# Performance work log

Hardware: AMD Instinct MI355X
Metric: run time of the kernel (lower is better)

Reference implementation:

```python
import jax, jax.numpy as jnp
import numpy as np

N_NODES = 20000  # number of atoms (scatter target count)


def setup_inputs() -> dict:
    key = jax.random.key(0)
    ks = jax.random.split(key, 7)
    E, F, R, L, O = 640000, 128, 16, 3, 12
    return {
        "m_ji": jax.random.normal(ks[0], (E, F), jnp.float32),
        "rbf_ji": jax.random.normal(ks[1], (E, R), jnp.float32),
        "atom_edge_index": jax.random.randint(ks[2], (2, E), 0, N_NODES, jnp.int64),
        "W_rbf": jax.random.normal(ks[3], (F, R), jnp.float32) * (1.0 / np.sqrt(R)),
        "dense_W": jax.random.normal(ks[4], (L, F, F), jnp.float32) * (1.0 / np.sqrt(F)),
        "dense_b": jax.random.normal(ks[5], (L, F), jnp.float32) * 0.01,
        "W_out": jax.random.normal(ks[6], (O, F), jnp.float32) * (1.0 / np.sqrt(F)),
    }


def reference(m_ji, rbf_ji, atom_edge_index, W_rbf, dense_W, dense_b, W_out):
    # e_ji = lin_rbf(rbf_ji): [E, dim_rbf] @ [dim_rbf, F] -> [E, F]
    e_ji = jnp.einsum("er,fr->ef", rbf_ji, W_rbf)
    # elementwise gate
    message_ji = e_ji * m_ji
    # scatter-add messages onto receiving atoms (index row 1)
    atom_i = jax.ops.segment_sum(message_ji, atom_edge_index[1], num_segments=N_NODES)
    # dense MLP stack with SiLU activation
    num_lin = dense_W.shape[0]
    for idx in range(num_lin):
        atom_i = jax.nn.silu(jnp.einsum("nf,gf->ng", atom_i, dense_W[idx]) + dense_b[idx])
    # final bias-free projection
    return jnp.einsum("nf,of->no", atom_i, W_out)
```

## Files before the change

kernel.cpp:

```cpp
#include <hip/hip_runtime.h>
#include <math.h>

#define F 128
#define R 16
#define O 12
#define NB 32
#define EB 16

__global__ void zero_int_kernel(int* __restrict__ p, int n) {
    int i = blockIdx.x * blockDim.x + threadIdx.x;
    if (i < n) p[i] = 0;
}

__global__ __launch_bounds__(256) void hist_kernel(
    const int* __restrict__ idx, int* __restrict__ cnt, int E)
{
    int i = blockIdx.x * blockDim.x + threadIdx.x;
    int stride = gridDim.x * blockDim.x;
    for (; i < E; i += stride) atomicAdd(&cnt[idx[i]], 1);
}

__global__ __launch_bounds__(1024) void scan_kernel(
    const int* __restrict__ cnt, int* __restrict__ off,
    int* __restrict__ cur, int N, int E)
{
    __shared__ int part[1024];
    int t = threadIdx.x;
    const int per = (N + 1023) / 1024;
    int s0 = t * per;
    int s = 0;
    for (int i = 0; i < per; i++) { int k = s0 + i; if (k < N) s += cnt[k]; }
    part[t] = s;
    __syncthreads();
    for (int d = 1; d < 1024; d <<= 1) {
        int v = (t >= d) ? part[t - d] : 0;
        __syncthreads();
        part[t] += v;
        __syncthreads();
    }
    int run = (t == 0) ? 0 : part[t - 1];
    for (int i = 0; i < per; i++) {
        int k = s0 + i;
        if (k < N) { off[k] = run; cur[k] = run; run += cnt[k]; }
    }
    if (t == 0) off[N] = E;
}

__global__ __launch_bounds__(256) void fill_kernel(
    const int* __restrict__ idx, int* __restrict__ cur,
    int* __restrict__ csr, int E)
{
    int i = blockIdx.x * blockDim.x + threadIdx.x;
    int stride = gridDim.x * blockDim.x;
    for (; i < E; i += stride) {
        int n = idx[i];
        int p = atomicAdd(&cur[n], 1);
        csr[p] = i;
    }
}

__device__ __forceinline__ float dot16(const float4* r, const float4* Wv) {
    float s = 0.f;
    #pragma unroll
    for (int q = 0; q < 4; q++)
        s += r[q].x * Wv[q].x + r[q].y * Wv[q].y + r[q].z * Wv[q].z + r[q].w * Wv[q].w;
    return s;
}

__device__ __forceinline__ void gld_lds16(const float* g, float* l) {
    __builtin_amdgcn_global_load_lds(
        (const __attribute__((address_space(1))) void*)g,
        (__attribute__((address_space(3))) void*)l,
        16, 0, 0);
}

__global__ __launch_bounds__(256) void gather_kernel(
    const float* __restrict__ m, const float* __restrict__ rbf,
    const int* __restrict__ csr, const int* __restrict__ off,
    const float* __restrict__ Wrbf, float* __restrict__ A, int N)
{
    __shared__ float m_buf[4 * EB * F];
    __shared__ float r_buf[4 * EB * R];
    const int lane = threadIdx.x & 63;
    const int w = threadIdx.x >> 6;
    const int n = blockIdx.x * 4 + w;
    if (n >= N) return;

    float* mw = m_buf + w * EB * F;
    float* rw = r_buf + w * EB * R;

    const int f0 = lane << 1;
    float4 W0[4], W1[4];
    #pragma unroll
    for (int q = 0; q < 4; q++) {
        W0[q] = *(const float4*)(Wrbf + (size_t)f0 * R + q * 4);
        W1[q] = *(const float4*)(Wrbf + (size_t)(f0 + 1) * R + q * 4);
    }

    float a0 = 0.f, a1 = 0.f;
    const int jb = off[n], je = off[n + 1];

    for (int j = jb; j < je; j += EB) {
        const int c = (je - j < EB) ? (je - j) : EB;

        asm volatile("s_waitcnt lgkmcnt(0)" ::: "memory");

        #pragma unroll
        for (int k = 0; k < EB / 2; k++) {
            if (2 * k < c) {
                int jj = j + 2 * k + (lane >> 5);
                if (jj > je - 1) jj = je - 1;
                int e = csr[jj];
                gld_lds16(m + (size_t)e * F + ((lane & 31) << 2), mw + k * 2 * F);
            }
        }
        {
            int jj = j + (lane >> 2);
            if (jj > je - 1) jj = je - 1;
            int e = csr[jj];
            gld_lds16(rbf + (size_t)e * R + ((lane & 3) << 2), rw);
        }

        asm volatile("s_waitcnt vmcnt(0)" ::: "memory");

        for (int r = 0; r < c; r++) {
            float2 mv = *(const float2*)(mw + r * F + f0);
            const float4* rr = (const float4*)(rw + r * R);
            float4 rv[4] = { rr[0], rr[1], rr[2], rr[3] };
            a0 += dot16(rv, W0) * mv.x;
            a1 += dot16(rv, W1) * mv.y;
        }
    }

    *(float2*)(A + (size_t)n * F + f0) = make_float2(a0, a1);
}

__global__ __launch_bounds__(256) void mlp_fused(
    const float* __restrict__ A, const float* __restrict__ dW,
    const float* __restrict__ db, const float* __restrict__ Wout,
    float* __restrict__ out, int N)
{
    __shared__ float Ws[F * F];
    __shared__ float act[NB * F];
    int t = threadIdx.x;
    int base = blockIdx.x * NB;
    int j = t & 15, i = t >> 4;

    int  n0[2]; bool ok[2];
    #pragma unroll
    for (int k = 0; k < 2; k++) { n0[k] = base + i + 16 * k; ok[k] = n0[k] < N; }

    for (int l = 0; l < 3; l++) {
        __syncthreads();
        for (int s = t; s < F * F / 4; s += 256) {
            int g = s >> 5, c = s & 31;
            float4 v = *(const float4*)(dW + (size_t)l * F * F + g * F + (c << 2));
            *(float4*)(Ws + g * F + ((c ^ (g & 31)) << 2)) = v;
        }
        __syncthreads();

        float acc[2][8];
        #pragma unroll
        for (int k = 0; k < 2; k++)
            #pragma unroll
            for (int mm = 0; mm < 8; mm++) acc[k][mm] = 0.f;

        for (int c = 0; c < 32; c++) {
            int f = c << 2;
            float4 av[2];
            #pragma unroll
            for (int k = 0; k < 2; k++) {
                if (l == 0)
                    av[k] = ok[k] ? *(const float4*)(A + (size_t)n0[k] * F + f)
                                  : make_float4(0.f, 0.f, 0.f, 0.f);
                else
                    av[k] = *(const float4*)(act + (i + 16 * k) * F + f);
            }
            float4 wv[8];
            #pragma unroll
            for (int mm = 0; mm < 8; mm++) {
                int g = j + 16 * mm;
                wv[mm] = *(const float4*)(Ws + g * F + ((c ^ (g & 31)) << 2));
            }
            #pragma unroll
            for (int k = 0; k < 2; k++)
                #pragma unroll
                for (int mm = 0; mm < 8; mm++)
                    acc[k][mm] += av[k].x * wv[mm].x + av[k].y * wv[mm].y +
                                  av[k].z * wv[mm].z + av[k].w * wv[mm].w;
        }

        #pragma unroll
        for (int mm = 0; mm < 8; mm++) {
            int g = j + 16 * mm;
            float bias = db[l * F + g];
            #pragma unroll
            for (int k = 0; k < 2; k++) {
                float x = acc[k][mm] + bias;
                act[(i + 16 * k) * F + g] = x / (1.f + __expf(-x));
            }
        }
    }

    __syncthreads();
    for (int s = t; s < O * F / 4; s += 256)
        ((float4*)Ws)[s] = ((const float4*)Wout)[s];
    __syncthreads();

    int nl = t >> 3;
    int oq = t & 7;
    int n = base + nl;
    if (n < N) {
        float s0 = 0.f, s1 = 0.f;
        for (int f = 0; f < F; f += 4) {
            float4 a  = *(const float4*)(act + nl * F + f);
            float4 w0 = *(const float4*)(Ws + oq * F + f);
            s0 += a.x * w0.x + a.y * w0.y + a.z * w0.z + a.w * w0.w;
            if (oq < 4) {
                float4 w1 = *(const float4*)(Ws + (8 + oq) * F + f);
                s1 += a.x * w1.x + a.y * w1.y + a.z * w1.z + a.w * w1.w;
            }
        }
        out[(size_t)n * O + oq] = s0;
        if (oq < 4) out[(size_t)n * O + 8 + oq] = s1;
    }
}

extern "C" void kernel_launch(void* const* d_in, const int* in_sizes, int n_in,
                              void* d_out, int out_size, void* d_ws, size_t ws_size,
                              hipStream_t stream)
{
    const float* m    = (const float*)d_in[0];
    const float* rbf  = (const float*)d_in[1];
    const int*   aei  = (const int*)d_in[2];
    const float* Wrbf = (const float*)d_in[3];
    const float* dW   = (const float*)d_in[4];
    const float* db   = (const float*)d_in[5];
    const float* Wout = (const float*)d_in[6];
    float* out = (float*)d_out;

    int E = in_sizes[0] / F;
    int N = out_size / O;

    float* A = (float*)d_ws;
    int* csr = (int*)(A + (size_t)N * F);
    int* cnt = csr + E;
    int* cur = cnt + N;
    int* off = cur + N;

    const int* idx1 = aei + E;

    zero_int_kernel<<<(N + 255) / 256, 256, 0, stream>>>(cnt, N);
    hist_kernel<<<1024, 256, 0, stream>>>(idx1, cnt, E);
    scan_kernel<<<1, 1024, 0, stream>>>(cnt, off, cur, N, E);
    fill_kernel<<<1024, 256, 0, stream>>>(idx1, cur, csr, E);
    gather_kernel<<<(N + 3) / 4, 256, 0, stream>>>(m, rbf, csr, off, Wrbf, A, N);

    mlp_fused<<<(N + NB - 1) / NB, 256, 0, stream>>>(A, dW, db, Wout, out, N);
}
```

Baseline: 743.4 us.

## Double-buffer edge message gathers and load rbf rows via scalar broadcast

The gather kernel now double-buffers the per-wave LDS staging of m rows. The next chunk's CSR indices are read into scalar registers and their async global-to-LDS loads are issued before the current chunk is processed. rbf rows are no longer staged through LDS; each lane loads them directly from uniform addresses, prefetching one row ahead in registers. The chunk size drops to 8 to keep LDS use the same. The aim is to hide gather latency behind compute. The cost is more vector registers, more uniform global loads, and partial vmcnt waits that must match the number of outstanding loads.

```diff
diff --git a/kernel.cpp b/kernel.cpp
--- a/kernel.cpp
+++ b/kernel.cpp
@@ -5,7 +5,7 @@
 #define R 16
 #define O 12
 #define NB 32
-#define EB 16
+#define EB 8
 
 __global__ void zero_int_kernel(int* __restrict__ p, int n) {
     int i = blockIdx.x * blockDim.x + threadIdx.x;
@@ -79,15 +79,13 @@
     const int* __restrict__ csr, const int* __restrict__ off,
     const float* __restrict__ Wrbf, float* __restrict__ A, int N)
 {
-    __shared__ float m_buf[4 * EB * F];
-    __shared__ float r_buf[4 * EB * R];
+    __shared__ float m_buf[4 * 2 * EB * F];
     const int lane = threadIdx.x & 63;
     const int w = threadIdx.x >> 6;
     const int n = blockIdx.x * 4 + w;
     if (n >= N) return;
 
-    float* mw = m_buf + w * EB * F;
-    float* rw = r_buf + w * EB * R;
+    float* mw = m_buf + w * (2 * EB * F);
 
     const int f0 = lane << 1;
     float4 W0[4], W1[4];
@@ -99,36 +97,72 @@
 
     float a0 = 0.f, a1 = 0.f;
     const int jb = off[n], je = off[n + 1];
-
-    for (int j = jb; j < je; j += EB) {
-        const int c = (je - j < EB) ? (je - j) : EB;
-
-        asm volatile("s_waitcnt lgkmcnt(0)" ::: "memory");
+    const int last = je - 1;
+
+    if (jb < je) {
+        int ec[EB], en[EB];
+        #pragma unroll
+        for (int k = 0; k < EB; k++) {
+            int jj = jb + k; if (jj > last) jj = last;
+            ec[k] = __builtin_amdgcn_readfirstlane(csr[jj]);
+        }
+        #pragma unroll
+        for (int k = 0; k < EB; k++) en[k] = ec[k];
 
         #pragma unroll
         for (int k = 0; k < EB / 2; k++) {
-            if (2 * k < c) {
-                int jj = j + 2 * k + (lane >> 5);
-                if (jj > je - 1) jj = je - 1;
-                int e = csr[jj];
-                gld_lds16(m + (size_t)e * F + ((lane & 31) << 2), mw + k * 2 * F);
-            }
-        }
-        {
-            int jj = j + (lane >> 2);
-            if (jj > je - 1) jj = je - 1;
-            int e = csr[jj];
-            gld_lds16(rbf + (size_t)e * R + ((lane & 3) << 2), rw);
-        }
-
-        asm volatile("s_waitcnt vmcnt(0)" ::: "memory");
-
-        for (int r = 0; r < c; r++) {
-            float2 mv = *(const float2*)(mw + r * F + f0);
-            const float4* rr = (const float4*)(rw + r * R);
-            float4 rv[4] = { rr[0], rr[1], rr[2], rr[3] };
-            a0 += dot16(rv, W0) * mv.x;
-            a1 += dot16(rv, W1) * mv.y;
+            int e = (lane < 32) ? ec[2 * k] : ec[2 * k + 1];
+            gld_lds16(m + (size_t)e * F + ((lane & 31) << 2), mw + k * 2 * F);
+        }
+
+        int buf = 0;
+        for (int j0 = jb; j0 < je; j0 += EB) {
+            const int c = (je - j0 < EB) ? (je - j0) : EB;
+            const int jn = j0 + EB;
+            const bool more = (jn < je);
+
+            if (more) {
+                #pragma unroll
+                for (int k = 0; k < EB; k++) {
+                    int jj = jn + k; if (jj > last) jj = last;
+                    en[k] = __builtin_amdgcn_readfirstlane(csr[jj]);
+                }
+                asm volatile("s_waitcnt lgkmcnt(0)" ::: "memory");
+                float* dst = mw + (buf ^ 1) * EB * F;
+                #pragma unroll
+                for (int k = 0; k < EB / 2; k++) {
+                    int e = (lane < 32) ? en[2 * k] : en[2 * k + 1];
+                    gld_lds16(m + (size_t)e * F + ((lane & 31) << 2), dst + k * 2 * F);
+                }
+                asm volatile("s_waitcnt vmcnt(4)" ::: "memory");
+            } else {
+                asm volatile("s_waitcnt vmcnt(0)" ::: "memory");
+            }
+
+            const float* src = mw + buf * EB * F;
+
+            float4 ra[4], rb[4];
+            {
+                const float4* p = (const float4*)(rbf + (size_t)ec[0] * R);
+                ra[0] = p[0]; ra[1] = p[1]; ra[2] = p[2]; ra[3] = p[3];
+            }
+            #pragma unroll
+            for (int r = 0; r < EB; r++) {
+                if (r >= c) break;
+                {
+                    const float4* p = (const float4*)(rbf + (size_t)ec[(r + 1) & (EB - 1)] * R);
+                    float4* nxt = (r & 1) ? ra : rb;
+                    nxt[0] = p[0]; nxt[1] = p[1]; nxt[2] = p[2]; nxt[3] = p[3];
+                }
+                const float4* cur4 = (r & 1) ? rb : ra;
+                float2 mv = *(const float2*)(src + r * F + f0);
+                a0 += dot16(cur4, W0) * mv.x;
+                a1 += dot16(cur4, W1) * mv.y;
+            }
+
+            #pragma unroll
+            for (int k = 0; k < EB; k++) ec[k] = en[k];
+            buf ^= 1;
         }
     }
 
```

New measurement: 823.2 us. 1.11x slower.
